# Kernel optimization log

Measured on AMD Instinct MI355X. Metric: run time of the kernel, lower is better.

Reference implementation:

```python
import jax, jax.numpy as jnp
import numpy as np

N_HEADS = 16

def setup_inputs() -> dict:
    key = jax.random.key(0)
    ks = jax.random.split(key, 5)
    C = 1024
    B, T = 2, 2048
    s_in = 1.0 / np.sqrt(C)
    x = jax.random.normal(ks[0], (B, T, C), dtype=jnp.float32)
    W_qkv = jax.random.normal(ks[1], (C, 3 * C), dtype=jnp.float32) * s_in
    b_qkv = jnp.zeros((3 * C,), dtype=jnp.float32)
    W_proj = jax.random.normal(ks[2], (C, C), dtype=jnp.float32) * s_in
    b_proj = jnp.zeros((C,), dtype=jnp.float32)
    return {"x": x, "W_qkv": W_qkv, "b_qkv": b_qkv, "W_proj": W_proj, "b_proj": b_proj}

def reference(x, W_qkv, b_qkv, W_proj, b_proj):
    B, T, C = x.shape
    H = N_HEADS
    D = C // H  # head dim
    qkv = x @ W_qkv + b_qkv                      # [B,T,3C]
    q, k, v = jnp.split(qkv, 3, axis=-1)
    # [B,T,C] -> [B,H,T,D]
    q = q.reshape(B, T, H, D).transpose(0, 2, 1, 3)
    k = k.reshape(B, T, H, D).transpose(0, 2, 1, 3)
    v = v.reshape(B, T, H, D).transpose(0, 2, 1, 3)
    scale = 1.0 / np.sqrt(D)
    att = jnp.einsum('bhqd,bhkd->bhqk', q, k) * scale  # [B,H,T,T]
    causal = jnp.tril(jnp.ones((T, T), dtype=bool))
    att = jnp.where(causal[None, None], att, -jnp.inf)
    att = jax.nn.softmax(att, axis=-1)
    y = jnp.einsum('bhqk,bhkd->bhqd', att, v)    # [B,H,T,D]
    y = y.transpose(0, 2, 1, 3).reshape(B, T, C)
    return y @ W_proj + b_proj
```

## Files before the change

kernel.cpp:

```cpp
#include <hip/hip_runtime.h>
#include <hip/hip_bf16.h>
#include <stdint.h>

#define DEVI __device__ __forceinline__

typedef __attribute__((ext_vector_type(8))) short bf16x8;
typedef __attribute__((ext_vector_type(4))) float f32x4;
typedef __attribute__((ext_vector_type(4))) short short4v;
typedef __attribute__((ext_vector_type(4))) float float4v;
typedef __attribute__((ext_vector_type(2))) unsigned int uint2v;

#define QSCALE 0.1803368801111204f

DEVI unsigned short f2bf(float f) {
  union { float f; unsigned u; } v; v.f = f;
  unsigned r = v.u + 0x7FFFu + ((v.u >> 16) & 1u);
  return (unsigned short)(r >> 16);
}

DEVI unsigned cvt_pk_bf16(float lo, float hi) {
  unsigned r;
  asm("v_cvt_pk_bf16_f32 %0, %1, %2" : "=v"(r) : "v"(lo), "v"(hi));
  return r;
}

DEVI void async16(unsigned short* lds, const unsigned short* g) {
  __builtin_amdgcn_global_load_lds(
      (const __attribute__((address_space(1))) void*)g,
      (__attribute__((address_space(3))) void*)lds, 16, 0, 0);
}

DEVI int xcd_swz_flat() {
  int orig = (int)blockIdx.x + (int)gridDim.x * (int)blockIdx.y;
  int cpx = ((int)gridDim.x * (int)gridDim.y) >> 3;
  return (orig & 7) * cpx + (orig >> 3);
}

__global__ void k_f32_to_bf16(const float* __restrict__ in,
                              unsigned short* __restrict__ out, int n4) {
  int i = blockIdx.x * 256 + threadIdx.x;
  if (i < n4) {
    float4v f = *reinterpret_cast<const float4v*>(in + (size_t)i * 4);
    short4v o;
#pragma unroll
    for (int j = 0; j < 4; ++j) o[j] = (short)f2bf(f[j]);
    *reinterpret_cast<short4v*>(out + (size_t)i * 4) = o;
  }
}

__global__ void k_wt(const float* __restrict__ W, unsigned short* __restrict__ Wt,
                     int K, int N) {
  __shared__ float tile[32][33];
  int n0 = blockIdx.x * 32, k0 = blockIdx.y * 32;
  int r = threadIdx.x >> 5, c = threadIdx.x & 31;
#pragma unroll
  for (int i = 0; i < 4; ++i)
    tile[r + i * 8][c] = W[(size_t)(k0 + r + i * 8) * N + n0 + c];
  __syncthreads();
#pragma unroll
  for (int i = 0; i < 4; ++i)
    Wt[(size_t)(n0 + r + i * 8) * K + k0 + c] = f2bf(tile[c][r + i * 8]);
}

DEVI void stage_ab(unsigned short* AsB, unsigned short* BsB,
                   const unsigned short* Ab, const unsigned short* Bb,
                   int K, int k0, int tid) {
#pragma unroll
  for (int it = 0; it < 2; ++it) {
    int c = it * 256 + tid;
    int row = c >> 2, cc = (c & 3) * 8;
    async16(&AsB[c * 8], Ab + (size_t)row * K + k0 + cc);
    async16(&BsB[c * 8], Bb + (size_t)row * K + k0 + cc);
  }
}

template <int EPI>
__global__ void k_gemm(const unsigned short* __restrict__ A,
                       const unsigned short* __restrict__ Bt,
                       const float* __restrict__ bias,
                       void* __restrict__ outp, int M, int N, int K) {
  __shared__ __align__(16) unsigned short As[2][128 * 32];
  __shared__ __align__(16) unsigned short Bs[2][128 * 32];
  const int tid = threadIdx.x;
  const int swzf = xcd_swz_flat();
  const int m0 = (swzf / (int)gridDim.x) * 128, n0 = (swzf % (int)gridDim.x) * 128;
  const int lane = tid & 63, w = tid >> 6;
  const int wr = (w >> 1) * 64, wc = (w & 1) * 64;
  const int lr = lane & 15, lg = lane >> 4;
  f32x4 acc[4][4] = {};
  const unsigned short* Ab = A + (size_t)m0 * K;
  const unsigned short* Bb = Bt + (size_t)n0 * K;

  const int ns = K >> 5;
  stage_ab(As[0], Bs[0], Ab, Bb, K, 0, tid);
  stage_ab(As[1], Bs[1], Ab, Bb, K, 32, tid);
  asm volatile("s_waitcnt vmcnt(4)" ::: "memory");
  __builtin_amdgcn_s_barrier();
  __builtin_amdgcn_sched_barrier(0);

  for (int s = 0; s < ns; ++s) {
    const int cur = s & 1;
    bf16x8 af[4], bfr[4];
#pragma unroll
    for (int m = 0; m < 4; ++m)
      af[m] = *reinterpret_cast<const bf16x8*>(&As[cur][(wr + m * 16 + lr) * 32 + lg * 8]);
#pragma unroll
    for (int n = 0; n < 4; ++n)
      bfr[n] = *reinterpret_cast<const bf16x8*>(&Bs[cur][(wc + n * 16 + lr) * 32 + lg * 8]);
#pragma unroll
    for (int m = 0; m < 4; ++m)
#pragma unroll
      for (int n = 0; n < 4; ++n)
        acc[m][n] = __builtin_amdgcn_mfma_f32_16x16x32_bf16(af[m], bfr[n], acc[m][n], 0, 0, 0);
    __builtin_amdgcn_s_barrier();
    const int ks = (s + 2 < ns) ? (s + 2) * 32 : 0;
    stage_ab(As[cur], Bs[cur], Ab, Bb, K, ks, tid);
    asm volatile("s_waitcnt vmcnt(4)" ::: "memory");
    __builtin_amdgcn_s_barrier();
    __builtin_amdgcn_sched_barrier(0);
  }
  if (EPI == 0) {
    unsigned short* qkv = (unsigned short*)outp;
#pragma unroll
    for (int n = 0; n < 4; ++n) {
      int col = n0 + wc + n * 16 + lr;
      float bv = bias[col];
      int sel = col >> 10, cc = col & 1023;
      int h = cc >> 6, d = cc & 63;
      float sc = (sel == 0) ? QSCALE : 1.0f;
#pragma unroll
      for (int m = 0; m < 4; ++m) {
#pragma unroll
        for (int r = 0; r < 4; ++r) {
          int row = m0 + wr + m * 16 + lg * 4 + r;
          int bh = ((row >> 11) << 4) + h;
          int t = row & 2047;
          qkv[((size_t)(sel * 32 + bh) * 2048 + t) * 64 + d] = f2bf((acc[m][n][r] + bv) * sc);
        }
      }
    }
  } else {
    float* O = (float*)outp;
#pragma unroll
    for (int n = 0; n < 4; ++n) {
      int col = n0 + wc + n * 16 + lr;
      float bv = bias[col];
#pragma unroll
      for (int m = 0; m < 4; ++m)
#pragma unroll
        for (int r = 0; r < 4; ++r) {
          int row = m0 + wr + m * 16 + lg * 4 + r;
          O[(size_t)row * N + col] = acc[m][n][r] + bv;
        }
    }
  }
}

__global__ __launch_bounds__(256)
void k_gemmP(const unsigned short* __restrict__ A,
             const unsigned short* __restrict__ Bt,
             const float* __restrict__ bias,
             float* __restrict__ O, int M, int N, int K) {
  __shared__ __align__(16) unsigned short As[2][128 * 32];
  __shared__ __align__(16) unsigned short Bs[2][64 * 32];
  const int tid = threadIdx.x;
  const int swzf = xcd_swz_flat();
  const int m0 = (swzf / (int)gridDim.x) * 128, n0 = (swzf % (int)gridDim.x) * 64;
  const int lane = tid & 63, w = tid >> 6;
  const int wr = (w >> 1) * 64, wc = (w & 1) * 32;
  const int lr = lane & 15, lg = lane >> 4;
  f32x4 acc[4][2] = {};
  const unsigned short* Ab = A + (size_t)m0 * K;
  const unsigned short* Bb = Bt + (size_t)n0 * K;

  auto stage = [&](unsigned short* AsB, unsigned short* BsB, int k0) {
#pragma unroll
    for (int it = 0; it < 2; ++it) {
      int c = it * 256 + tid;
      int row = c >> 2, cc = (c & 3) * 8;
      async16(&AsB[c * 8], Ab + (size_t)row * K + k0 + cc);
    }
    int row = tid >> 2, cc = (tid & 3) * 8;
    async16(&BsB[tid * 8], Bb + (size_t)row * K + k0 + cc);
  };

  const int ns = K >> 5;
  stage(As[0], Bs[0], 0);
  stage(As[1], Bs[1], 32);
  asm volatile("s_waitcnt vmcnt(3)" ::: "memory");
  __builtin_amdgcn_s_barrier();
  __builtin_amdgcn_sched_barrier(0);

  for (int s = 0; s < ns; ++s) {
    const int cur = s & 1;
    bf16x8 af[4], bfr[2];
#pragma unroll
    for (int m = 0; m < 4; ++m)
      af[m] = *reinterpret_cast<const bf16x8*>(&As[cur][(wr + m * 16 + lr) * 32 + lg * 8]);
#pragma unroll
    for (int n = 0; n < 2; ++n)
      bfr[n] = *reinterpret_cast<const bf16x8*>(&Bs[cur][(wc + n * 16 + lr) * 32 + lg * 8]);
#pragma unroll
    for (int m = 0; m < 4; ++m)
#pragma unroll
      for (int n = 0; n < 2; ++n)
        acc[m][n] = __builtin_amdgcn_mfma_f32_16x16x32_bf16(af[m], bfr[n], acc[m][n], 0, 0, 0);
    __builtin_amdgcn_s_barrier();
    const int ks = (s + 2 < ns) ? (s + 2) * 32 : 0;
    stage(As[cur], Bs[cur], ks);
    asm volatile("s_waitcnt vmcnt(3)" ::: "memory");
    __builtin_amdgcn_s_barrier();
    __builtin_amdgcn_sched_barrier(0);
  }
#pragma unroll
  for (int n = 0; n < 2; ++n) {
    int col = n0 + wc + n * 16 + lr;
    float bv = bias[col];
#pragma unroll
    for (int m = 0; m < 4; ++m)
#pragma unroll
      for (int r = 0; r < 4; ++r) {
        int row = m0 + wr + m * 16 + lg * 4 + r;
        O[(size_t)row * N + col] = acc[m][n][r] + bv;
      }
  }
}

__global__ void k_vt(const unsigned short* __restrict__ V,
                     unsigned short* __restrict__ Vt) {
  __shared__ __align__(16) unsigned short t[64][72];
  int bh = blockIdx.y, t0 = blockIdx.x * 64;
  int r = threadIdx.x >> 3, c8 = (threadIdx.x & 7) * 8;
#pragma unroll
  for (int i = 0; i < 2; ++i) {
    int row = i * 32 + r;
    *reinterpret_cast<bf16x8*>(&t[row][c8]) =
        *reinterpret_cast<const bf16x8*>(&V[((size_t)bh * 2048 + t0 + row) * 64 + c8]);
  }
  __syncthreads();
#pragma unroll
  for (int i = 0; i < 2; ++i) {
    int d = i * 32 + r;
    bf16x8 o;
#pragma unroll
    for (int j = 0; j < 8; ++j) o[j] = (short)t[c8 + j][d];
    *reinterpret_cast<bf16x8*>(&Vt[((size_t)bh * 64 + d) * 2048 + t0 + c8]) = o;
  }
}

DEVI void stage_kv(unsigned short* KsB, unsigned short* VsB,
                   const unsigned short* Kbh, const unsigned short* Vbh,
                   int k0, int tid, int srow, int gcol) {
  async16(&KsB[tid * 8], Kbh + (size_t)(k0 + srow) * 64 + gcol);
  async16(&VsB[tid * 8], Vbh + (size_t)srow * 2048 + k0 + gcol);
}

DEVI void attn_store(unsigned short* __restrict__ Y, int bh, int qw, int lg, int lr,
                     const f32x4* o, float l_run) {
  const int b = bh >> 4, h = bh & 15;
  float rl = 1.0f / l_run;
  float rlo[4];
#pragma unroll
  for (int r = 0; r < 4; ++r) rlo[r] = __shfl(rl, lg * 4 + r, 64);
#pragma unroll
  for (int r = 0; r < 4; ++r) {
    int t = qw + lg * 4 + r;
#pragma unroll
    for (int n = 0; n < 4; ++n)
      Y[((size_t)(b * 2048 + t)) * 1024 + h * 64 + n * 16 + lr] = f2bf(o[n][r] * rlo[r]);
  }
}

__global__ __launch_bounds__(512)
void k_attn(const unsigned short* __restrict__ Qg,
            const unsigned short* __restrict__ Kg,
            const unsigned short* __restrict__ Vtg,
            unsigned short* __restrict__ Y) {
  __shared__ __align__(16) unsigned short Ks[2][64 * 64];
  __shared__ __align__(16) unsigned short Vs[2][64 * 64];
  __shared__ __align__(16) unsigned short Ps[8][16 * 64];
  const int orig = (int)blockIdx.x;
  const int slot = orig >> 8;
  const int within = orig & 255;
  const int sw = (within & 7) * 32 + (within >> 3);
  const int bh = sw >> 3;
  const int xp = sw & 7;
  const int x = slot ? xp : (15 - xp);
  const int nkt = 2 * x + 2;
  const int tid = threadIdx.x, lane = tid & 63, w = tid >> 6;
  const int lr = lane & 15, lg = lane >> 4;
  const int swz = (lane & 7) * 8;
  const int psw = (lr & 7) * 8;
  const unsigned short* Kbh = Kg + (size_t)bh * 2048 * 64;
  const unsigned short* Vbh = Vtg + (size_t)bh * 64 * 2048;

  const int qw = x * 128 + w * 16;
  const unsigned short* Qrow = Qg + ((size_t)bh * 2048 + qw + lr) * 64;
  bf16x8 qa0 = *reinterpret_cast<const bf16x8*>(&Qrow[lg * 8]);
  bf16x8 qa1 = *reinterpret_cast<const bf16x8*>(&Qrow[32 + lg * 8]);

  float m_run = -1e30f, l_run = 0.f;
  f32x4 o[4] = {};

  const int srow = tid >> 3;
  const int gcol = ((tid & 7) ^ (srow & 7)) * 8;

  stage_kv(Ks[0], Vs[0], Kbh, Vbh, 0, tid, srow, gcol);
  stage_kv(Ks[1], Vs[1], Kbh, Vbh, 64, tid, srow, gcol);
  asm volatile("s_waitcnt vmcnt(2)" ::: "memory");
  __builtin_amdgcn_s_barrier();
  __builtin_amdgcn_sched_barrier(0);

  for (int t = 0; t < nkt; ++t) {
    const int cur = t & 1;
    const int k0 = t * 64;
    if (k0 <= qw + 15) {
      const unsigned short* KsC = Ks[cur];
      const unsigned short* VsC = Vs[cur];

      f32x4 s[4];
      __builtin_amdgcn_s_setprio(1);
#pragma unroll
      for (int n = 0; n < 4; ++n) {
        bf16x8 kb0 = *reinterpret_cast<const bf16x8*>(&KsC[(n * 16 + lr) * 64 + ((lg * 8) ^ swz)]);
        bf16x8 kb1 = *reinterpret_cast<const bf16x8*>(&KsC[(n * 16 + lr) * 64 + ((32 + lg * 8) ^ swz)]);
        f32x4 z = {0.f, 0.f, 0.f, 0.f};
        z = __builtin_amdgcn_mfma_f32_16x16x32_bf16(kb0, qa0, z, 0, 0, 0);
        z = __builtin_amdgcn_mfma_f32_16x16x32_bf16(kb1, qa1, z, 0, 0, 0);
        s[n] = z;
      }
      __builtin_amdgcn_s_setprio(0);
      if (k0 + 63 > qw) {
        const int klim = qw + lr - k0 - lg * 4;
#pragma unroll
        for (int n = 0; n < 4; ++n)
#pragma unroll
          for (int r = 0; r < 4; ++r)
            if (n * 16 + r > klim) s[n][r] = -1e30f;
      }
      float tmax = s[0][0];
#pragma unroll
      for (int n = 0; n < 4; ++n)
#pragma unroll
        for (int r = 0; r < 4; ++r) tmax = fmaxf(tmax, s[n][r]);
      tmax = fmaxf(tmax, __shfl_xor(tmax, 16, 64));
      tmax = fmaxf(tmax, __shfl_xor(tmax, 32, 64));
      if (__any(tmax > m_run + 11.5f)) {
        float mNew = fmaxf(m_run, tmax);
        float alpha = __builtin_exp2f(m_run - mNew);
        m_run = mNew;
        l_run *= alpha;
        float ao[4];
#pragma unroll
        for (int r = 0; r < 4; ++r) ao[r] = __shfl(alpha, lg * 4 + r, 64);
#pragma unroll
        for (int n = 0; n < 4; ++n)
#pragma unroll
          for (int r = 0; r < 4; ++r) o[n][r] *= ao[r];
      }
      float tsum = 0.f;
#pragma unroll
      for (int n = 0; n < 4; ++n)
#pragma unroll
        for (int r = 0; r < 4; ++r) {
          s[n][r] = __builtin_exp2f(s[n][r] - m_run);
          tsum += s[n][r];
        }
      tsum += __shfl_xor(tsum, 16, 64);
      tsum += __shfl_xor(tsum, 32, 64);
      l_run += tsum;
#pragma unroll
      for (int n = 0; n < 4; ++n) {
        uint2v pk;
        pk[0] = cvt_pk_bf16(s[n][0], s[n][1]);
        pk[1] = cvt_pk_bf16(s[n][2], s[n][3]);
        *reinterpret_cast<uint2v*>(&Ps[w][lr * 64 + ((n * 16 + lg * 4) ^ psw)]) = pk;
      }
      __builtin_amdgcn_s_setprio(1);
#pragma unroll
      for (int jj = 0; jj < 2; ++jj) {
        bf16x8 pa = *reinterpret_cast<const bf16x8*>(&Ps[w][lr * 64 + ((jj * 32 + lg * 8) ^ psw)]);
#pragma unroll
        for (int n = 0; n < 4; ++n) {
          bf16x8 vb = *reinterpret_cast<const bf16x8*>(
              &VsC[(n * 16 + lr) * 64 + ((jj * 32 + lg * 8) ^ swz)]);
          o[n] = __builtin_amdgcn_mfma_f32_16x16x32_bf16(pa, vb, o[n], 0, 0, 0);
        }
      }
      __builtin_amdgcn_s_setprio(0);
    }
    __builtin_amdgcn_s_barrier();
    {
      const int ts = (t + 2 < nkt) ? (t + 2) : 0;
      stage_kv(Ks[cur], Vs[cur], Kbh, Vbh, ts * 64, tid, srow, gcol);
    }
    asm volatile("s_waitcnt vmcnt(2)" ::: "memory");
    __builtin_amdgcn_s_barrier();
    __builtin_amdgcn_sched_barrier(0);
  }
  attn_store(Y, bh, qw, lg, lr, o, l_run);
}

extern "C" void kernel_launch(void* const* d_in, const int* in_sizes, int n_in,
                              void* d_out, int out_size, void* d_ws, size_t ws_size,
                              hipStream_t stream) {
  const float* x     = (const float*)d_in[0];
  const float* Wqkv  = (const float*)d_in[1];
  const float* bqkv  = (const float*)d_in[2];
  const float* Wproj = (const float*)d_in[3];
  const float* bproj = (const float*)d_in[4];
  float* out = (float*)d_out;

  uint8_t* ws = (uint8_t*)d_ws;
  unsigned short* xb     = (unsigned short*)(ws);
  unsigned short* wqkvT  = (unsigned short*)(ws + ((size_t)8  << 20));
  unsigned short* wprojT = (unsigned short*)(ws + ((size_t)14 << 20));
  unsigned short* qkvb   = (unsigned short*)(ws + ((size_t)16 << 20));
  unsigned short* vt     = (unsigned short*)(ws + ((size_t)40 << 20));

  k_f32_to_bf16<<<4096, 256, 0, stream>>>(x, xb, 1048576);
  k_wt<<<dim3(96, 32), 256, 0, stream>>>(Wqkv, wqkvT, 1024, 3072);
  k_wt<<<dim3(32, 32), 256, 0, stream>>>(Wproj, wprojT, 1024, 1024);
  k_gemm<0><<<dim3(24, 32), 256, 0, stream>>>(xb, wqkvT, bqkv, qkvb, 4096, 3072, 1024);
  k_vt<<<dim3(32, 32), 256, 0, stream>>>(qkvb + (size_t)2 * 32 * 2048 * 64, vt);
  k_attn<<<dim3(512, 1), 512, 0, stream>>>(qkvb, qkvb + (size_t)32 * 2048 * 64, vt, xb);
  k_gemmP<<<dim3(16, 32), 256, 0, stream>>>(xb, wprojT, bproj, out, 4096, 1024, 1024);
}
```

Before: 123.3 us.

## Fuse V transpose into QKV GEMM, merge weight casts, use 128-key attention tiles

```diff
diff --git a/kernel.cpp b/kernel.cpp
--- a/kernel.cpp
+++ b/kernel.cpp
@@ -48,10 +48,16 @@
   }
 }
 
-__global__ void k_wt(const float* __restrict__ W, unsigned short* __restrict__ Wt,
-                     int K, int N) {
+__global__ void k_wt2(const float* __restrict__ Wq, const float* __restrict__ Wp,
+                      unsigned short* __restrict__ WqT, unsigned short* __restrict__ WpT) {
   __shared__ float tile[32][33];
-  int n0 = blockIdx.x * 32, k0 = blockIdx.y * 32;
+  const int bx = (int)blockIdx.x;
+  const float* W;
+  unsigned short* Wt;
+  int N, n0;
+  if (bx < 96) { W = Wq; Wt = WqT; N = 3072; n0 = bx * 32; }
+  else         { W = Wp; Wt = WpT; N = 1024; n0 = (bx - 96) * 32; }
+  const int K = 1024, k0 = (int)blockIdx.y * 32;
   int r = threadIdx.x >> 5, c = threadIdx.x & 31;
 #pragma unroll
   for (int i = 0; i < 4; ++i)
@@ -74,11 +80,12 @@
   }
 }
 
-template <int EPI>
 __global__ void k_gemm(const unsigned short* __restrict__ A,
                        const unsigned short* __restrict__ Bt,
                        const float* __restrict__ bias,
-                       void* __restrict__ outp, int M, int N, int K) {
+                       unsigned short* __restrict__ qkv,
+                       unsigned short* __restrict__ vt,
+                       int M, int N, int K) {
   __shared__ __align__(16) unsigned short As[2][128 * 32];
   __shared__ __align__(16) unsigned short Bs[2][128 * 32];
   const int tid = threadIdx.x;
@@ -119,14 +126,13 @@
     __builtin_amdgcn_s_barrier();
     __builtin_amdgcn_sched_barrier(0);
   }
-  if (EPI == 0) {
-    unsigned short* qkv = (unsigned short*)outp;
-#pragma unroll
-    for (int n = 0; n < 4; ++n) {
-      int col = n0 + wc + n * 16 + lr;
-      float bv = bias[col];
-      int sel = col >> 10, cc = col & 1023;
-      int h = cc >> 6, d = cc & 63;
+#pragma unroll
+  for (int n = 0; n < 4; ++n) {
+    int col = n0 + wc + n * 16 + lr;
+    float bv = bias[col];
+    int sel = col >> 10, cc = col & 1023;
+    int h = cc >> 6, d = cc & 63;
+    if (sel < 2) {
       float sc = (sel == 0) ? QSCALE : 1.0f;
 #pragma unroll
       for (int m = 0; m < 4; ++m) {
@@ -138,20 +144,17 @@
           qkv[((size_t)(sel * 32 + bh) * 2048 + t) * 64 + d] = f2bf((acc[m][n][r] + bv) * sc);
         }
       }
-    }
-  } else {
-    float* O = (float*)outp;
-#pragma unroll
-    for (int n = 0; n < 4; ++n) {
-      int col = n0 + wc + n * 16 + lr;
-      float bv = bias[col];
-#pragma unroll
-      for (int m = 0; m < 4; ++m)
-#pragma unroll
-        for (int r = 0; r < 4; ++r) {
-          int row = m0 + wr + m * 16 + lg * 4 + r;
-          O[(size_t)row * N + col] = acc[m][n][r] + bv;
-        }
+    } else {
+#pragma unroll
+      for (int m = 0; m < 4; ++m) {
+        int row0 = m0 + wr + m * 16 + lg * 4;
+        int bh = ((row0 >> 11) << 4) + h;
+        int t0 = row0 & 2047;
+        short4v pk;
+#pragma unroll
+        for (int r = 0; r < 4; ++r) pk[r] = (short)f2bf(acc[m][n][r] + bv);
+        *reinterpret_cast<short4v*>(&vt[((size_t)(bh * 64 + d)) * 2048 + t0]) = pk;
+      }
     }
   }
 }
@@ -226,33 +229,17 @@
   }
 }
 
-__global__ void k_vt(const unsigned short* __restrict__ V,
-                     unsigned short* __restrict__ Vt) {
-  __shared__ __align__(16) unsigned short t[64][72];
-  int bh = blockIdx.y, t0 = blockIdx.x * 64;
-  int r = threadIdx.x >> 3, c8 = (threadIdx.x & 7) * 8;
-#pragma unroll
-  for (int i = 0; i < 2; ++i) {
-    int row = i * 32 + r;
-    *reinterpret_cast<bf16x8*>(&t[row][c8]) =
-        *reinterpret_cast<const bf16x8*>(&V[((size_t)bh * 2048 + t0 + row) * 64 + c8]);
-  }
-  __syncthreads();
-#pragma unroll
-  for (int i = 0; i < 2; ++i) {
-    int d = i * 32 + r;
-    bf16x8 o;
-#pragma unroll
-    for (int j = 0; j < 8; ++j) o[j] = (short)t[c8 + j][d];
-    *reinterpret_cast<bf16x8*>(&Vt[((size_t)bh * 64 + d) * 2048 + t0 + c8]) = o;
-  }
-}
-
 DEVI void stage_kv(unsigned short* KsB, unsigned short* VsB,
                    const unsigned short* Kbh, const unsigned short* Vbh,
-                   int k0, int tid, int srow, int gcol) {
-  async16(&KsB[tid * 8], Kbh + (size_t)(k0 + srow) * 64 + gcol);
-  async16(&VsB[tid * 8], Vbh + (size_t)srow * 2048 + k0 + gcol);
+                   int k0, int tid) {
+#pragma unroll
+  for (int i = 0; i < 2; ++i) {
+    int c = i * 512 + tid;
+    int krow = c >> 3, kcc = c & 7;
+    async16(&KsB[c * 8], Kbh + (size_t)(k0 + krow) * 64 + ((kcc ^ (krow & 7)) * 8));
+    int vrow = c >> 4, vcc = c & 15;
+    async16(&VsB[c * 8], Vbh + (size_t)vrow * 2048 + k0 + ((vcc ^ (vrow & 7)) * 8));
+  }
 }
 
 DEVI void attn_store(unsigned short* __restrict__ Y, int bh, int qw, int lg, int lr,
@@ -276,8 +263,8 @@
             const unsigned short* __restrict__ Kg,
             const unsigned short* __restrict__ Vtg,
             unsigned short* __restrict__ Y) {
-  __shared__ __align__(16) unsigned short Ks[2][64 * 64];
-  __shared__ __align__(16) unsigned short Vs[2][64 * 64];
+  __shared__ __align__(16) unsigned short Ks[2][128 * 64];
+  __shared__ __align__(16) unsigned short Vs[2][64 * 128];
   __shared__ __align__(16) unsigned short Ps[8][16 * 64];
   const int orig = (int)blockIdx.x;
   const int slot = orig >> 8;
@@ -286,11 +273,10 @@
   const int bh = sw >> 3;
   const int xp = sw & 7;
   const int x = slot ? xp : (15 - xp);
-  const int nkt = 2 * x + 2;
+  const int nkt = x + 1;
   const int tid = threadIdx.x, lane = tid & 63, w = tid >> 6;
   const int lr = lane & 15, lg = lane >> 4;
   const int swz = (lane & 7) * 8;
-  const int psw = (lr & 7) * 8;
   const unsigned short* Kbh = Kg + (size_t)bh * 2048 * 64;
   const unsigned short* Vbh = Vtg + (size_t)bh * 64 * 2048;
 
@@ -302,26 +288,33 @@
   float m_run = -1e30f, l_run = 0.f;
   f32x4 o[4] = {};
 
-  const int srow = tid >> 3;
-  const int gcol = ((tid & 7) ^ (srow & 7)) * 8;
-
-  stage_kv(Ks[0], Vs[0], Kbh, Vbh, 0, tid, srow, gcol);
-  stage_kv(Ks[1], Vs[1], Kbh, Vbh, 64, tid, srow, gcol);
-  asm volatile("s_waitcnt vmcnt(2)" ::: "memory");
+  stage_kv(Ks[0], Vs[0], Kbh, Vbh, 0, tid);
+  stage_kv(Ks[1], Vs[1], Kbh, Vbh, (nkt > 1) ? 128 : 0, tid);
+  asm volatile("s_waitcnt vmcnt(4)" ::: "memory");
   __builtin_amdgcn_s_barrier();
   __builtin_amdgcn_sched_barrier(0);
 
   for (int t = 0; t < nkt; ++t) {
     const int cur = t & 1;
-    const int k0 = t * 64;
-    if (k0 <= qw + 15) {
-      const unsigned short* KsC = Ks[cur];
-      const unsigned short* VsC = Vs[cur];
-
-      f32x4 s[4];
-      __builtin_amdgcn_s_setprio(1);
-#pragma unroll
-      for (int n = 0; n < 4; ++n) {
+    const int k0 = t * 128;
+    const unsigned short* KsC = Ks[cur];
+    const unsigned short* VsC = Vs[cur];
+    const bool full = (k0 + 64 <= qw + 15);
+
+    f32x4 s[8];
+    __builtin_amdgcn_s_setprio(1);
+#pragma unroll
+    for (int n = 0; n < 4; ++n) {
+      bf16x8 kb0 = *reinterpret_cast<const bf16x8*>(&KsC[(n * 16 + lr) * 64 + ((lg * 8) ^ swz)]);
+      bf16x8 kb1 = *reinterpret_cast<const bf16x8*>(&KsC[(n * 16 + lr) * 64 + ((32 + lg * 8) ^ swz)]);
+      f32x4 z = {0.f, 0.f, 0.f, 0.f};
+      z = __builtin_amdgcn_mfma_f32_16x16x32_bf16(kb0, qa0, z, 0, 0, 0);
+      z = __builtin_amdgcn_mfma_f32_16x16x32_bf16(kb1, qa1, z, 0, 0, 0);
+      s[n] = z;
+    }
+    if (full) {
+#pragma unroll
+      for (int n = 4; n < 8; ++n) {
         bf16x8 kb0 = *reinterpret_cast<const bf16x8*>(&KsC[(n * 16 + lr) * 64 + ((lg * 8) ^ swz)]);
         bf16x8 kb1 = *reinterpret_cast<const bf16x8*>(&KsC[(n * 16 + lr) * 64 + ((32 + lg * 8) ^ swz)]);
         f32x4 z = {0.f, 0.f, 0.f, 0.f};
@@ -329,61 +322,87 @@
         z = __builtin_amdgcn_mfma_f32_16x16x32_bf16(kb1, qa1, z, 0, 0, 0);
         s[n] = z;
       }
-      __builtin_amdgcn_s_setprio(0);
-      if (k0 + 63 > qw) {
-        const int klim = qw + lr - k0 - lg * 4;
-#pragma unroll
-        for (int n = 0; n < 4; ++n)
+    }
+    __builtin_amdgcn_s_setprio(0);
+    if (k0 + 127 > qw) {
+      const int klim = qw + lr - k0 - lg * 4;
+#pragma unroll
+      for (int n = 0; n < 4; ++n)
+#pragma unroll
+        for (int r = 0; r < 4; ++r)
+          if (n * 16 + r > klim) s[n][r] = -1e30f;
+      if (full) {
+#pragma unroll
+        for (int n = 4; n < 8; ++n)
 #pragma unroll
           for (int r = 0; r < 4; ++r)
             if (n * 16 + r > klim) s[n][r] = -1e30f;
       }
-      float tmax = s[0][0];
+    }
+    float tmax = s[0][0];
+#pragma unroll
+    for (int n = 0; n < 4; ++n)
+#pragma unroll
+      for (int r = 0; r < 4; ++r) tmax = fmaxf(tmax, s[n][r]);
+    if (full) {
+#pragma unroll
+      for (int n = 4; n < 8; ++n)
+#pragma unroll
+        for (int r = 0; r < 4; ++r) tmax = fmaxf(tmax, s[n][r]);
+    }
+    tmax = fmaxf(tmax, __shfl_xor(tmax, 16, 64));
+    tmax = fmaxf(tmax, __shfl_xor(tmax, 32, 64));
+    if (__any(tmax > m_run + 11.5f)) {
+      float mNew = fmaxf(m_run, tmax);
+      float alpha = __builtin_exp2f(m_run - mNew);
+      m_run = mNew;
+      l_run *= alpha;
+      float ao[4];
+#pragma unroll
+      for (int r = 0; r < 4; ++r) ao[r] = __shfl(alpha, lg * 4 + r, 64);
 #pragma unroll
       for (int n = 0; n < 4; ++n)
 #pragma unroll
-        for (int r = 0; r < 4; ++r) tmax = fmaxf(tmax, s[n][r]);
-      tmax = fmaxf(tmax, __shfl_xor(tmax, 16, 64));
-      tmax = fmaxf(tmax, __shfl_xor(tmax, 32, 64));
-      if (__any(tmax > m_run + 11.5f)) {
-        float mNew = fmaxf(m_run, tmax);
-        float alpha = __builtin_exp2f(m_run - mNew);
-        m_run = mNew;
-        l_run *= alpha;
-        float ao[4];
-#pragma unroll
-        for (int r = 0; r < 4; ++r) ao[r] = __shfl(alpha, lg * 4 + r, 64);
-#pragma unroll
-        for (int n = 0; n < 4; ++n)
-#pragma unroll
-          for (int r = 0; r < 4; ++r) o[n][r] *= ao[r];
-      }
-      float tsum = 0.f;
-#pragma unroll
-      for (int n = 0; n < 4; ++n)
+        for (int r = 0; r < 4; ++r) o[n][r] *= ao[r];
+    }
+    float tsum = 0.f;
+#pragma unroll
+    for (int n = 0; n < 4; ++n)
+#pragma unroll
+      for (int r = 0; r < 4; ++r) {
+        s[n][r] = __builtin_exp2f(s[n][r] - m_run);
+        tsum += s[n][r];
+      }
+    if (full) {
+#pragma unroll
+      for (int n = 4; n < 8; ++n)
 #pragma unroll
         for (int r = 0; r < 4; ++r) {
           s[n][r] = __builtin_exp2f(s[n][r] - m_run);
           tsum += s[n][r];
         }
-      tsum += __shfl_xor(tsum, 16, 64);
-      tsum += __shfl_xor(tsum, 32, 64);
-      l_run += tsum;
-#pragma unroll
-      for (int n = 0; n < 4; ++n) {
+    }
+    tsum += __shfl_xor(tsum, 16, 64);
+    tsum += __shfl_xor(tsum, 32, 64);
+    l_run += tsum;
+#pragma unroll
+    for (int hh = 0; hh < 2; ++hh) {
+      if (hh == 1 && !full) break;
+#pragma unroll
+      for (int n2 = 0; n2 < 4; ++n2) {
         uint2v pk;
-        pk[0] = cvt_pk_bf16(s[n][0], s[n][1]);
-        pk[1] = cvt_pk_bf16(s[n][2], s[n][3]);
-        *reinterpret_cast<uint2v*>(&Ps[w][lr * 64 + ((n * 16 + lg * 4) ^ psw)]) = pk;
+        pk[0] = cvt_pk_bf16(s[hh * 4 + n2][0], s[hh * 4 + n2][1]);
+        pk[1] = cvt_pk_bf16(s[hh * 4 + n2][2], s[hh * 4 + n2][3]);
+        *reinterpret_cast<uint2v*>(&Ps[w][lr * 64 + ((n2 * 16 + lg * 4) ^ swz)]) = pk;
       }
       __builtin_amdgcn_s_setprio(1);
 #pragma unroll
       for (int jj = 0; jj < 2; ++jj) {
-        bf16x8 pa = *reinterpret_cast<const bf16x8*>(&Ps[w][lr * 64 + ((jj * 32 + lg * 8) ^ psw)]);
+        bf16x8 pa = *reinterpret_cast<const bf16x8*>(&Ps[w][lr * 64 + ((jj * 32 + lg * 8) ^ swz)]);
 #pragma unroll
         for (int n = 0; n < 4; ++n) {
           bf16x8 vb = *reinterpret_cast<const bf16x8*>(
-              &VsC[(n * 16 + lr) * 64 + ((jj * 32 + lg * 8) ^ swz)]);
+              &VsC[(n * 16 + lr) * 128 + ((hh * 64 + jj * 32 + lg * 8) ^ swz)]);
           o[n] = __builtin_amdgcn_mfma_f32_16x16x32_bf16(pa, vb, o[n], 0, 0, 0);
         }
       }
@@ -392,9 +411,9 @@
     __builtin_amdgcn_s_barrier();
     {
       const int ts = (t + 2 < nkt) ? (t + 2) : 0;
-      stage_kv(Ks[cur], Vs[cur], Kbh, Vbh, ts * 64, tid, srow, gcol);
-    }
-    asm volatile("s_waitcnt vmcnt(2)" ::: "memory");
+      stage_kv(Ks[cur], Vs[cur], Kbh, Vbh, ts * 128, tid);
+    }
+    asm volatile("s_waitcnt vmcnt(4)" ::: "memory");
     __builtin_amdgcn_s_barrier();
     __builtin_amdgcn_sched_barrier(0);
   }
@@ -416,13 +435,11 @@
   unsigned short* wqkvT  = (unsigned short*)(ws + ((size_t)8  << 20));
   unsigned short* wprojT = (unsigned short*)(ws + ((size_t)14 << 20));
   unsigned short* qkvb   = (unsigned short*)(ws + ((size_t)16 << 20));
-  unsigned short* vt     = (unsigned short*)(ws + ((size_t)40 << 20));
+  unsigned short* vt     = (unsigned short*)(ws + ((size_t)32 << 20));
 
   k_f32_to_bf16<<<4096, 256, 0, stream>>>(x, xb, 1048576);
-  k_wt<<<dim3(96, 32), 256, 0, stream>>>(Wqkv, wqkvT, 1024, 3072);
-  k_wt<<<dim3(32, 32), 256, 0, stream>>>(Wproj, wprojT, 1024, 1024);
-  k_gemm<0><<<dim3(24, 32), 256, 0, stream>>>(xb, wqkvT, bqkv, qkvb, 4096, 3072, 1024);
-  k_vt<<<dim3(32, 32), 256, 0, stream>>>(qkvb + (size_t)2 * 32 * 2048 * 64, vt);
+  k_wt2<<<dim3(128, 32), 256, 0, stream>>>(Wqkv, Wproj, wqkvT, wprojT);
+  k_gemm<<<dim3(24, 32), 256, 0, stream>>>(xb, wqkvT, bqkv, qkvb, vt, 4096, 3072, 1024);
   k_attn<<<dim3(512, 1), 512, 0, stream>>>(qkvb, qkvb + (size_t)32 * 2048 * 64, vt, xb);
   k_gemmP<<<dim3(16, 32), 256, 0, stream>>>(xb, wprojT, bproj, out, 4096, 1024, 1024);
 }
```

After: 129.5 us. +5.0%, slower.
